# Kernel optimization log

Hardware: AMD Instinct MI355X
Metric: run time of the kernel (lower is better)

Reference implementation:

```python
import jax, jax.numpy as jnp
import numpy as np

N = 100000
E = 1600000
IN_C, HID_C, OUT_C = 128, 128, 64


def setup_inputs() -> dict:
    key = jax.random.key(0)
    k1, k2, k3, k4 = jax.random.split(key, 4)
    x = jax.random.normal(k1, (N, IN_C), dtype=jnp.float32)
    edge_index = jax.random.randint(k2, (2, E), 0, N, dtype=jnp.int32)
    # Glorot-ish scaled weights
    W1 = jax.random.normal(k3, (IN_C, HID_C), dtype=jnp.float32) / np.sqrt(IN_C)
    b1 = jnp.zeros((HID_C,), dtype=jnp.float32)
    W2 = jax.random.normal(k4, (HID_C, OUT_C), dtype=jnp.float32) / np.sqrt(HID_C)
    b2 = jnp.zeros((OUT_C,), dtype=jnp.float32)
    return {"x": x, "edge_index": edge_index, "W1": W1, "b1": b1, "W2": W2, "b2": b2}


def _gcn_norm(edge_index, num_nodes):
    """Add self loops and compute symmetric D^{-1/2} A D^{-1/2} edge weights (PyG GCNConv defaults)."""
    loop = jnp.arange(num_nodes, dtype=edge_index.dtype)
    row = jnp.concatenate([edge_index[0], loop])  # source nodes
    col = jnp.concatenate([edge_index[1], loop])  # target nodes
    ones = jnp.ones_like(col, dtype=jnp.float32)
    deg = jax.ops.segment_sum(ones, col, num_segments=num_nodes)
    deg_inv_sqrt = jnp.where(deg > 0, jax.lax.rsqrt(jnp.maximum(deg, 1.0)), 0.0)
    norm = deg_inv_sqrt[row] * deg_inv_sqrt[col]  # [E+N]
    return row, col, norm


def _gcn_layer(x, row, col, norm, W, b, num_nodes):
    h = x @ W                                   # [N, C_out] transform first (PyG order)
    msg = h[row] * norm[:, None]                # gather + scale  [E+N, C_out]
    out = jax.ops.segment_sum(msg, col, num_segments=num_nodes)  # scatter-add
    return out + b


def reference(x, edge_index, W1, b1, W2, b2):
    row, col, norm = _gcn_norm(edge_index, N)
    h = jax.nn.relu(_gcn_layer(x, row, col, norm, W1, b1, N))
    return _gcn_layer(h, row, col, norm, W2, b2, N)
```

## Files before the change

kernel.cpp:

```cpp
#include <hip/hip_runtime.h>
#include <hip/hip_fp16.h>

#define NODES 100000
#define EDGES 1600000

#define BSHIFT 9
#define BNODES 512
#define NBUCK ((NODES + BNODES - 1) / BNODES)
#define BCAP 10240

typedef __attribute__((ext_vector_type(8))) short short8;
typedef __attribute__((ext_vector_type(4))) float f32x4;

__device__ inline unsigned short f2bf(float f) {
    unsigned u = __builtin_bit_cast(unsigned, f);
    u = u + 0x7fff + ((u >> 16) & 1);
    return (unsigned short)(u >> 16);
}
__device__ inline float bf2f(unsigned short h) {
    unsigned u = ((unsigned)h) << 16;
    return __builtin_bit_cast(float, u);
}
__device__ inline unsigned short f2h_bits(float f) {
    __half h = __float2half_rn(f);
    return __builtin_bit_cast(unsigned short, h);
}
__device__ inline float h2f(unsigned short bits) {
    return __half2float(__builtin_bit_cast(__half, bits));
}
__device__ inline float2 h2f2(unsigned int bits) {
    __half2 h = __builtin_bit_cast(__half2, bits);
    return __half22float2(h);
}


__global__ __launch_bounds__(1024) void bucket_scatter(const int* __restrict__ row,
                                                       const int* __restrict__ col,
                                                       int* __restrict__ gcur,
                                                       int2* __restrict__ temp) {
    __shared__ int hist[NBUCK];
    __shared__ int base[NBUCK];
    const int tid = threadIdx.x;
    for (int i = tid; i < NBUCK; i += 1024) hist[i] = 0;
    __syncthreads();

    const int e = blockIdx.x * 1024 + tid;
    const bool valid = e < EDGES;
    int b = 0, rank = 0, src = 0, c = 0;
    if (valid) {
        c = col[e];
        src = row[e];
        b = c >> BSHIFT;
        rank = atomicAdd(&hist[b], 1);
    }
    __syncthreads();
    for (int i = tid; i < NBUCK; i += 1024) {
        int h = hist[i];
        base[i] = h ? atomicAdd(&gcur[i], h) : 0;
    }
    __syncthreads();
    if (valid) {
        int pos = base[b] + rank;
        int2 v;
        v.x = src;
        v.y = c & (BNODES - 1);
        temp[(size_t)b * BCAP + pos] = v;
    }
}

__global__ __launch_bounds__(256) void bucket_scan(const int* __restrict__ gcur,
                                                   int* __restrict__ bbase,
                                                   int* __restrict__ row_start) {
    __shared__ int s[256];
    const int t = threadIdx.x;
    int v = (t < NBUCK) ? gcur[t] : 0;
    s[t] = v;
    __syncthreads();
    for (int d = 1; d < 256; d <<= 1) {
        int x = (t >= d) ? s[t - d] : 0;
        __syncthreads();
        s[t] += x;
        __syncthreads();
    }
    if (t < NBUCK) bbase[t] = s[t] - v;
    if (t == 0) row_start[NODES] = EDGES;
}

__global__ __launch_bounds__(1024) void bucket_build(const int2* __restrict__ temp,
                                                     const int* __restrict__ gcur,
                                                     const int* __restrict__ bbase,
                                                     int* __restrict__ row_start,
                                                     float* __restrict__ dis,
                                                     int* __restrict__ esrc) {
    __shared__ int cnt[BNODES];
    __shared__ int offs[BNODES];
    __shared__ int cur[BNODES];
    const int b = blockIdx.x;
    const int tid = threadIdx.x;
    const int size = gcur[b];
    const int gbase = bbase[b];

    if (tid < BNODES) cnt[tid] = 0;
    __syncthreads();

    for (int i = tid; i < size; i += 1024) {
        int2 v = temp[(size_t)b * BCAP + i];
        atomicAdd(&cnt[v.y], 1);
    }
    __syncthreads();

    if (tid < BNODES) offs[tid] = cnt[tid];
    __syncthreads();
    for (int d = 1; d < BNODES; d <<= 1) {
        int x = 0;
        if (tid < BNODES && tid >= d) x = offs[tid - d];
        __syncthreads();
        if (tid < BNODES) offs[tid] += x;
        __syncthreads();
    }
    if (tid < BNODES) {
        int excl = offs[tid] - cnt[tid];
        cur[tid] = excl;
        int v = b * BNODES + tid;
        if (v < NODES) {
            row_start[v] = gbase + excl;
            dis[v] = rsqrtf((float)(cnt[tid] + 1));
        }
    }
    __syncthreads();

    for (int i = tid; i < size; i += 1024) {
        int2 v = temp[(size_t)b * BCAP + i];
        int pos = gbase + atomicAdd(&cur[v.y], 1);
        esrc[pos] = v.x;
    }
}


template <int NCOL>
__global__ __launch_bounds__(256) void w_prep(const float* __restrict__ W,
                                              unsigned short* __restrict__ wh,
                                              unsigned short* __restrict__ wl) {
    constexpr int NCT = NCOL / 16;
    constexpr int FRAGS = 4 * NCT * 64;
    int idx = blockIdx.x * 256 + threadIdx.x;
    if (idx >= FRAGS) return;
    int lane = idx & 63;
    int rem = idx >> 6;
    int ct = rem % NCT;
    int kt = rem / NCT;
    int kbase = kt * 32 + ((lane >> 4) * 8);
    int c = ct * 16 + (lane & 15);
#pragma unroll
    for (int i = 0; i < 8; i++) {
        float v = W[(size_t)(kbase + i) * NCOL + c];
        unsigned short hi = f2bf(v);
        unsigned short lo = f2bf(v - bf2f(hi));
        wh[(size_t)idx * 8 + i] = hi;
        wl[(size_t)idx * 8 + i] = lo;
    }
}


template <int NCOL, bool IN_HALF>
__global__ __launch_bounds__(512) void gemm_mfma(const void* __restrict__ Xv,
                                                 const unsigned short* __restrict__ wh,
                                                 const unsigned short* __restrict__ wl,
                                                 const float* __restrict__ dis,
                                                 unsigned short* __restrict__ H) {
    constexpr int NCT = NCOL / 16;
    constexpr int FRAGS = 4 * NCT * 64;
    __shared__ unsigned short s_wh[FRAGS * 8];
    __shared__ unsigned short s_wl[FRAGS * 8];

    const int tid = threadIdx.x;
    const int wave = tid >> 6;
    const int lane = tid & 63;

    const int row0 = blockIdx.x * 128 + wave * 16 + (lane & 15);
    const bool active = (blockIdx.x * 128 + wave * 16) < NODES;

    float xs[4][8];
    if (active) {
        if constexpr (IN_HALF) {
            const unsigned short* xrow = (const unsigned short*)Xv + (size_t)row0 * 128 + ((lane >> 4) * 8);
#pragma unroll
            for (int kt = 0; kt < 4; kt++) {
                short8 raw = *(const short8*)(xrow + kt * 32);
#pragma unroll
                for (int i = 0; i < 8; i++) xs[kt][i] = h2f((unsigned short)raw[i]);
            }
        } else {
            const float* xrow = (const float*)Xv + (size_t)row0 * 128 + ((lane >> 4) * 8);
#pragma unroll
            for (int kt = 0; kt < 4; kt++) {
                float4 a = *(const float4*)(xrow + kt * 32);
                float4 b = *(const float4*)(xrow + kt * 32 + 4);
                xs[kt][0] = a.x; xs[kt][1] = a.y; xs[kt][2] = a.z; xs[kt][3] = a.w;
                xs[kt][4] = b.x; xs[kt][5] = b.y; xs[kt][6] = b.z; xs[kt][7] = b.w;
            }
        }
    }

    constexpr int ROUNDS = (FRAGS * 16) / (512 * 16);
#pragma unroll
    for (int j = 0; j < ROUNDS; j++) {
        __builtin_amdgcn_global_load_lds((const unsigned int*)((const char*)wh + ((size_t)tid + j * 512) * 16),
                                         (unsigned int*)(s_wh + ((size_t)tid + j * 512) * 8), 16, 0, 0);
        __builtin_amdgcn_global_load_lds((const unsigned int*)((const char*)wl + ((size_t)tid + j * 512) * 16),
                                         (unsigned int*)(s_wl + ((size_t)tid + j * 512) * 8), 16, 0, 0);
    }
    __syncthreads();

    if (!active) return;

    short8 ah[4], al[4];
#pragma unroll
    for (int kt = 0; kt < 4; kt++) {
#pragma unroll
        for (int i = 0; i < 8; i++) {
            unsigned short hi = f2bf(xs[kt][i]);
            unsigned short lo = f2bf(xs[kt][i] - bf2f(hi));
            ah[kt][i] = (short)hi;
            al[kt][i] = (short)lo;
        }
    }

    f32x4 acc[NCT];
#pragma unroll
    for (int ct = 0; ct < NCT; ct++) acc[ct] = (f32x4){0.f, 0.f, 0.f, 0.f};

#pragma unroll
    for (int kt = 0; kt < 4; kt++) {
#pragma unroll
        for (int ct = 0; ct < NCT; ct++) {
            const int fo = ((kt * NCT + ct) * 64 + lane) * 8;
            short8 bh = *(const short8*)&s_wh[fo];
            short8 bl = *(const short8*)&s_wl[fo];
            acc[ct] = __builtin_amdgcn_mfma_f32_16x16x32_bf16(ah[kt], bh, acc[ct], 0, 0, 0);
            acc[ct] = __builtin_amdgcn_mfma_f32_16x16x32_bf16(al[kt], bh, acc[ct], 0, 0, 0);
            acc[ct] = __builtin_amdgcn_mfma_f32_16x16x32_bf16(ah[kt], bl, acc[ct], 0, 0, 0);
        }
    }

    const int rbase = blockIdx.x * 128 + wave * 16 + ((lane >> 4) * 4);
    float d[4];
#pragma unroll
    for (int r = 0; r < 4; r++) d[r] = dis[rbase + r];
#pragma unroll
    for (int ct = 0; ct < NCT; ct++) {
#pragma unroll
        for (int r = 0; r < 4; r++) {
            H[(size_t)(rbase + r) * NCOL + ct * 16 + (lane & 15)] = f2h_bits(acc[ct][r] * d[r]);
        }
    }
}


template <int C, bool RELU, bool OUT_HALF>
__global__ __launch_bounds__(256, 8) void agg_v3(const unsigned short* __restrict__ H,
                                                 const int* __restrict__ row_start,
                                                 const int* __restrict__ edge_src,
                                                 const float* __restrict__ dis,
                                                 const float* __restrict__ bias,
                                                 void* __restrict__ OUT) {
    constexpr int GL = (C == 128) ? 16 : 8;
    constexpr int GPW = 64 / GL;
    constexpr int RQ = C / 8;

    const int lane = threadIdx.x & 63;
    const int sub = lane & (GL - 1);
    const int grp = lane >> ((C == 128) ? 4 : 3);
    const int wid = (blockIdx.x * 256 + threadIdx.x) >> 6;
    const int v = wid * GPW + grp;
    if (v >= NODES) return;

    const uint4* __restrict__ Hq = (const uint4*)H;

    const int e0 = row_start[v];
    const int e1 = row_start[v + 1];
    const float d = dis[v];

    const float4 ba = ((const float4*)bias)[sub * 2];
    const float4 bb = ((const float4*)bias)[sub * 2 + 1];

    uint4 gs = Hq[(size_t)v * RQ + sub];

    int i0 = edge_src[min(e0 + 0, EDGES - 1)];
    int i1 = edge_src[min(e0 + 1, EDGES - 1)];
    int i2 = edge_src[min(e0 + 2, EDGES - 1)];
    int i3 = edge_src[min(e0 + 3, EDGES - 1)];

    float a0, a1, a2, a3, a4, a5, a6, a7;
    {
        float2 f0 = h2f2(gs.x), f1 = h2f2(gs.y), f2 = h2f2(gs.z), f3 = h2f2(gs.w);
        a0 = f0.x; a1 = f0.y; a2 = f1.x; a3 = f1.y;
        a4 = f2.x; a5 = f2.y; a6 = f3.x; a7 = f3.y;
    }

    for (int k = e0; k < e1; k += 4) {
        uint4 g0 = Hq[(size_t)i0 * RQ + sub];
        uint4 g1 = Hq[(size_t)i1 * RQ + sub];
        uint4 g2 = Hq[(size_t)i2 * RQ + sub];
        uint4 g3 = Hq[(size_t)i3 * RQ + sub];
        i0 = edge_src[min(k + 4, EDGES - 1)];
        i1 = edge_src[min(k + 5, EDGES - 1)];
        i2 = edge_src[min(k + 6, EDGES - 1)];
        i3 = edge_src[min(k + 7, EDGES - 1)];
        const float w1 = (k + 1 < e1) ? 1.f : 0.f;
        const float w2 = (k + 2 < e1) ? 1.f : 0.f;
        const float w3 = (k + 3 < e1) ? 1.f : 0.f;
#define ACC(G, W)                                                        \
        {                                                                \
            float2 f0 = h2f2(G.x), f1 = h2f2(G.y);                       \
            float2 f2 = h2f2(G.z), f3 = h2f2(G.w);                       \
            a0 = fmaf(f0.x, W, a0); a1 = fmaf(f0.y, W, a1);              \
            a2 = fmaf(f1.x, W, a2); a3 = fmaf(f1.y, W, a3);              \
            a4 = fmaf(f2.x, W, a4); a5 = fmaf(f2.y, W, a5);              \
            a6 = fmaf(f3.x, W, a6); a7 = fmaf(f3.y, W, a7);              \
        }
        ACC(g0, 1.f)
        ACC(g1, w1)
        ACC(g2, w2)
        ACC(g3, w3)
#undef ACC
    }

    float o0 = fmaf(a0, d, ba.x);
    float o1 = fmaf(a1, d, ba.y);
    float o2 = fmaf(a2, d, ba.z);
    float o3 = fmaf(a3, d, ba.w);
    float o4 = fmaf(a4, d, bb.x);
    float o5 = fmaf(a5, d, bb.y);
    float o6 = fmaf(a6, d, bb.z);
    float o7 = fmaf(a7, d, bb.w);
    if constexpr (RELU) {
        o0 = fmaxf(o0, 0.f); o1 = fmaxf(o1, 0.f);
        o2 = fmaxf(o2, 0.f); o3 = fmaxf(o3, 0.f);
        o4 = fmaxf(o4, 0.f); o5 = fmaxf(o5, 0.f);
        o6 = fmaxf(o6, 0.f); o7 = fmaxf(o7, 0.f);
    }

    if constexpr (OUT_HALF) {
        uint4 o;
        o.x = __builtin_bit_cast(unsigned, __float22half2_rn(make_float2(o0, o1)));
        o.y = __builtin_bit_cast(unsigned, __float22half2_rn(make_float2(o2, o3)));
        o.z = __builtin_bit_cast(unsigned, __float22half2_rn(make_float2(o4, o5)));
        o.w = __builtin_bit_cast(unsigned, __float22half2_rn(make_float2(o6, o7)));
        ((uint4*)OUT)[(size_t)v * RQ + sub] = o;
    } else {
        float4 oa, ob;
        oa.x = o0; oa.y = o1; oa.z = o2; oa.w = o3;
        ob.x = o4; ob.y = o5; ob.z = o6; ob.w = o7;
        float* outp = (float*)OUT + (size_t)v * C + sub * 8;
        *(float4*)(outp) = oa;
        *(float4*)(outp + 4) = ob;
    }
}


extern "C" void kernel_launch(void* const* d_in, const int* in_sizes, int n_in,
                              void* d_out, int out_size, void* d_ws, size_t ws_size,
                              hipStream_t stream) {
    const float* x   = (const float*)d_in[0];
    const int* eidx  = (const int*)d_in[1];
    const float* W1  = (const float*)d_in[2];
    const float* b1  = (const float*)d_in[3];
    const float* W2  = (const float*)d_in[4];
    const float* b2  = (const float*)d_in[5];
    float* out = (float*)d_out;

    const int* erow = eidx;
    const int* ecol = eidx + EDGES;

    char* w = (char*)d_ws;
    size_t off = 0;
    auto alloc = [&](size_t bytes) -> void* {
        void* p = w + off;
        off += (bytes + 255) & ~(size_t)255;
        return p;
    };
    float* dis     = (float*)alloc((size_t)NODES * 4);
    int*   rowst   = (int*)alloc((size_t)(NODES + 1) * 4);
    int*   esrc    = (int*)alloc((size_t)EDGES * 4);
    int*   gcur    = (int*)alloc(NBUCK * 4);
    int*   bbase   = (int*)alloc(NBUCK * 4);
    int2*  temp    = (int2*)alloc((size_t)NBUCK * BCAP * 8);
    unsigned short* wh1 = (unsigned short*)alloc(2048 * 8 * 2);
    unsigned short* wl1 = (unsigned short*)alloc(2048 * 8 * 2);
    unsigned short* wh2 = (unsigned short*)alloc(1024 * 8 * 2);
    unsigned short* wl2 = (unsigned short*)alloc(1024 * 8 * 2);
    unsigned short* bufA = (unsigned short*)alloc((size_t)NODES * 128 * 2);
    unsigned short* bufB = (unsigned short*)alloc((size_t)NODES * 128 * 2);

    hipMemsetAsync(gcur, 0, NBUCK * 4, stream);

    bucket_scatter<<<(EDGES + 1023) / 1024, 1024, 0, stream>>>(erow, ecol, gcur, temp);
    bucket_scan<<<1, 256, 0, stream>>>(gcur, bbase, rowst);
    bucket_build<<<NBUCK, 1024, 0, stream>>>(temp, gcur, bbase, rowst, dis, esrc);

    w_prep<128><<<8, 256, 0, stream>>>(W1, wh1, wl1);
    w_prep<64><<<4, 256, 0, stream>>>(W2, wh2, wl2);

    const int GB = (NODES + 127) / 128;

    gemm_mfma<128, false><<<GB, 512, 0, stream>>>(x, wh1, wl1, dis, bufA);
    agg_v3<128, true, true><<<(NODES + 15) / 16, 256, 0, stream>>>(bufA, rowst, esrc, dis, b1, bufB);

    gemm_mfma<64, true><<<GB, 512, 0, stream>>>(bufB, wh2, wl2, dis, bufA);
    agg_v3<64, false, false><<<(NODES + 31) / 32, 256, 0, stream>>>(bufA, rowst, esrc, dis, b2, out);
}
```

Before: 195.2 us.

## Fuse layer-1 aggregation with layer-2 matmul and merge small prep kernels

Fuses the layer-1 aggregation (with bias and ReLU) and the layer-2 weight transform into one kernel. The aggregated row is staged in LDS and multiplied by an fp16 copy of W2 using scalar FMAs, replacing the separate MFMA GEMM and its extra round trip of the hidden activations through HBM. Weight prep and the gcur zeroing are merged into one kernel, and the bucket scan is folded into every bucket_build block, removing several launches and the memset. The cost is per-block redundant scans and a scalar-FMA matvec, with W2 held in fp16 instead of split bf16 hi/lo, which lowers precision.

```diff
diff --git a/kernel.cpp b/kernel.cpp
--- a/kernel.cpp
+++ b/kernel.cpp
@@ -11,6 +11,7 @@
 
 typedef __attribute__((ext_vector_type(8))) short short8;
 typedef __attribute__((ext_vector_type(4))) float f32x4;
+typedef unsigned short ushort_t;
 
 __device__ inline unsigned short f2bf(float f) {
     unsigned u = __builtin_bit_cast(unsigned, f);
@@ -31,6 +32,42 @@
 __device__ inline float2 h2f2(unsigned int bits) {
     __half2 h = __builtin_bit_cast(__half2, bits);
     return __half22float2(h);
+}
+
+
+__global__ __launch_bounds__(256) void prep_kernel(const float* __restrict__ W1,
+                                                   const float* __restrict__ W2,
+                                                   unsigned short* __restrict__ wh,
+                                                   unsigned short* __restrict__ wl,
+                                                   unsigned short* __restrict__ w2h,
+                                                   int* __restrict__ gcur) {
+    const int tid = threadIdx.x;
+    if (blockIdx.x < 8) {
+        constexpr int NCOL = 128;
+        constexpr int NCT = NCOL / 16;
+        int idx = blockIdx.x * 256 + tid;
+        int lane = idx & 63;
+        int rem = idx >> 6;
+        int ct = rem % NCT;
+        int kt = rem / NCT;
+        int kbase = kt * 32 + ((lane >> 4) * 8);
+        int c = ct * 16 + (lane & 15);
+#pragma unroll
+        for (int i = 0; i < 8; i++) {
+            float v = W1[(size_t)(kbase + i) * NCOL + c];
+            unsigned short hi = f2bf(v);
+            unsigned short lo = f2bf(v - bf2f(hi));
+            wh[(size_t)idx * 8 + i] = hi;
+            wl[(size_t)idx * 8 + i] = lo;
+        }
+    } else {
+#pragma unroll
+        for (int i = 0; i < 32; i++) {
+            int idx = i * 256 + tid;
+            w2h[idx] = f2h_bits(W2[idx]);
+        }
+        if (tid < NBUCK) gcur[tid] = 0;
+    }
 }
 
 
@@ -68,37 +105,29 @@
     }
 }
 
-__global__ __launch_bounds__(256) void bucket_scan(const int* __restrict__ gcur,
-                                                   int* __restrict__ bbase,
-                                                   int* __restrict__ row_start) {
-    __shared__ int s[256];
-    const int t = threadIdx.x;
-    int v = (t < NBUCK) ? gcur[t] : 0;
-    s[t] = v;
-    __syncthreads();
-    for (int d = 1; d < 256; d <<= 1) {
-        int x = (t >= d) ? s[t - d] : 0;
-        __syncthreads();
-        s[t] += x;
-        __syncthreads();
-    }
-    if (t < NBUCK) bbase[t] = s[t] - v;
-    if (t == 0) row_start[NODES] = EDGES;
-}
-
 __global__ __launch_bounds__(1024) void bucket_build(const int2* __restrict__ temp,
                                                      const int* __restrict__ gcur,
-                                                     const int* __restrict__ bbase,
                                                      int* __restrict__ row_start,
                                                      float* __restrict__ dis,
                                                      int* __restrict__ esrc) {
     __shared__ int cnt[BNODES];
     __shared__ int offs[BNODES];
     __shared__ int cur[BNODES];
+    __shared__ int ssc[256];
     const int b = blockIdx.x;
     const int tid = threadIdx.x;
+
+    if (tid < 256) ssc[tid] = (tid < NBUCK) ? gcur[tid] : 0;
+    __syncthreads();
+    for (int d = 1; d < 256; d <<= 1) {
+        int x = (tid < 256 && tid >= d) ? ssc[tid - d] : 0;
+        __syncthreads();
+        if (tid < 256) ssc[tid] += x;
+        __syncthreads();
+    }
     const int size = gcur[b];
-    const int gbase = bbase[b];
+    const int gbase = ssc[b] - size;
+    if (b == 0 && tid == 0) row_start[NODES] = EDGES;
 
     if (tid < BNODES) cnt[tid] = 0;
     __syncthreads();
@@ -137,37 +166,12 @@
 }
 
 
-template <int NCOL>
-__global__ __launch_bounds__(256) void w_prep(const float* __restrict__ W,
-                                              unsigned short* __restrict__ wh,
-                                              unsigned short* __restrict__ wl) {
-    constexpr int NCT = NCOL / 16;
-    constexpr int FRAGS = 4 * NCT * 64;
-    int idx = blockIdx.x * 256 + threadIdx.x;
-    if (idx >= FRAGS) return;
-    int lane = idx & 63;
-    int rem = idx >> 6;
-    int ct = rem % NCT;
-    int kt = rem / NCT;
-    int kbase = kt * 32 + ((lane >> 4) * 8);
-    int c = ct * 16 + (lane & 15);
-#pragma unroll
-    for (int i = 0; i < 8; i++) {
-        float v = W[(size_t)(kbase + i) * NCOL + c];
-        unsigned short hi = f2bf(v);
-        unsigned short lo = f2bf(v - bf2f(hi));
-        wh[(size_t)idx * 8 + i] = hi;
-        wl[(size_t)idx * 8 + i] = lo;
-    }
-}
-
-
-template <int NCOL, bool IN_HALF>
-__global__ __launch_bounds__(512) void gemm_mfma(const void* __restrict__ Xv,
+__global__ __launch_bounds__(512) void gemm_mfma(const float* __restrict__ X,
                                                  const unsigned short* __restrict__ wh,
                                                  const unsigned short* __restrict__ wl,
                                                  const float* __restrict__ dis,
                                                  unsigned short* __restrict__ H) {
+    constexpr int NCOL = 128;
     constexpr int NCT = NCOL / 16;
     constexpr int FRAGS = 4 * NCT * 64;
     __shared__ unsigned short s_wh[FRAGS * 8];
@@ -182,23 +186,13 @@
 
     float xs[4][8];
     if (active) {
-        if constexpr (IN_HALF) {
-            const unsigned short* xrow = (const unsigned short*)Xv + (size_t)row0 * 128 + ((lane >> 4) * 8);
-#pragma unroll
-            for (int kt = 0; kt < 4; kt++) {
-                short8 raw = *(const short8*)(xrow + kt * 32);
-#pragma unroll
-                for (int i = 0; i < 8; i++) xs[kt][i] = h2f((unsigned short)raw[i]);
-            }
-        } else {
-            const float* xrow = (const float*)Xv + (size_t)row0 * 128 + ((lane >> 4) * 8);
-#pragma unroll
-            for (int kt = 0; kt < 4; kt++) {
-                float4 a = *(const float4*)(xrow + kt * 32);
-                float4 b = *(const float4*)(xrow + kt * 32 + 4);
-                xs[kt][0] = a.x; xs[kt][1] = a.y; xs[kt][2] = a.z; xs[kt][3] = a.w;
-                xs[kt][4] = b.x; xs[kt][5] = b.y; xs[kt][6] = b.z; xs[kt][7] = b.w;
-            }
+        const float* xrow = X + (size_t)row0 * 128 + ((lane >> 4) * 8);
+#pragma unroll
+        for (int kt = 0; kt < 4; kt++) {
+            float4 a = *(const float4*)(xrow + kt * 32);
+            float4 b = *(const float4*)(xrow + kt * 32 + 4);
+            xs[kt][0] = a.x; xs[kt][1] = a.y; xs[kt][2] = a.z; xs[kt][3] = a.w;
+            xs[kt][4] = b.x; xs[kt][5] = b.y; xs[kt][6] = b.z; xs[kt][7] = b.w;
         }
     }
 
@@ -257,23 +251,138 @@
 }
 
 
-template <int C, bool RELU, bool OUT_HALF>
-__global__ __launch_bounds__(256, 8) void agg_v3(const unsigned short* __restrict__ H,
+__global__ __launch_bounds__(256) void agg_fused(const unsigned short* __restrict__ H,
+                                                 const int* __restrict__ row_start,
+                                                 const int* __restrict__ edge_src,
+                                                 const float* __restrict__ dis,
+                                                 const float* __restrict__ b1,
+                                                 const unsigned short* __restrict__ w2h,
+                                                 unsigned short* __restrict__ H2) {
+    __shared__ float h_lds[16][128];
+    __shared__ unsigned short w2_lds[128 * 64];
+
+    const int tid = threadIdx.x;
+    const int lane = tid & 63;
+    const int sub = lane & 15;
+    const int grp = lane >> 4;
+    const int nl = (tid >> 6) * 4 + grp;
+    const int v = blockIdx.x * 16 + nl;
+
+#pragma unroll
+    for (int j = 0; j < 4; j++) {
+        __builtin_amdgcn_global_load_lds((const unsigned int*)((const char*)w2h + ((size_t)tid + j * 256) * 16),
+                                         (unsigned int*)w2_lds + ((size_t)tid + j * 256) * 4, 16, 0, 0);
+    }
+
+    const uint4* __restrict__ Hq = (const uint4*)H;
+    const int e0 = row_start[v];
+    const int e1 = row_start[v + 1];
+    const float d = dis[v];
+
+    const float4 ba = ((const float4*)b1)[sub * 2];
+    const float4 bb = ((const float4*)b1)[sub * 2 + 1];
+
+    uint4 gs = Hq[(size_t)v * 16 + sub];
+
+    int i0 = edge_src[min(e0 + 0, EDGES - 1)];
+    int i1 = edge_src[min(e0 + 1, EDGES - 1)];
+    int i2 = edge_src[min(e0 + 2, EDGES - 1)];
+    int i3 = edge_src[min(e0 + 3, EDGES - 1)];
+
+    float a0, a1, a2, a3, a4, a5, a6, a7;
+    {
+        float2 f0 = h2f2(gs.x), f1 = h2f2(gs.y), f2 = h2f2(gs.z), f3 = h2f2(gs.w);
+        a0 = f0.x; a1 = f0.y; a2 = f1.x; a3 = f1.y;
+        a4 = f2.x; a5 = f2.y; a6 = f3.x; a7 = f3.y;
+    }
+
+    for (int k = e0; k < e1; k += 4) {
+        uint4 g0 = Hq[(size_t)i0 * 16 + sub];
+        uint4 g1 = Hq[(size_t)i1 * 16 + sub];
+        uint4 g2 = Hq[(size_t)i2 * 16 + sub];
+        uint4 g3 = Hq[(size_t)i3 * 16 + sub];
+        i0 = edge_src[min(k + 4, EDGES - 1)];
+        i1 = edge_src[min(k + 5, EDGES - 1)];
+        i2 = edge_src[min(k + 6, EDGES - 1)];
+        i3 = edge_src[min(k + 7, EDGES - 1)];
+        const float w1 = (k + 1 < e1) ? 1.f : 0.f;
+        const float w2 = (k + 2 < e1) ? 1.f : 0.f;
+        const float w3 = (k + 3 < e1) ? 1.f : 0.f;
+#define ACC(G, W)                                                        \
+        {                                                                \
+            float2 f0 = h2f2(G.x), f1 = h2f2(G.y);                       \
+            float2 f2 = h2f2(G.z), f3 = h2f2(G.w);                       \
+            a0 = fmaf(f0.x, W, a0); a1 = fmaf(f0.y, W, a1);              \
+            a2 = fmaf(f1.x, W, a2); a3 = fmaf(f1.y, W, a3);              \
+            a4 = fmaf(f2.x, W, a4); a5 = fmaf(f2.y, W, a5);              \
+            a6 = fmaf(f3.x, W, a6); a7 = fmaf(f3.y, W, a7);              \
+        }
+        ACC(g0, 1.f)
+        ACC(g1, w1)
+        ACC(g2, w2)
+        ACC(g3, w3)
+#undef ACC
+    }
+
+    {
+        float4 oa, ob;
+        oa.x = fmaf(a0, d, ba.x); oa.y = fmaf(a1, d, ba.y);
+        oa.z = fmaf(a2, d, ba.z); oa.w = fmaf(a3, d, ba.w);
+        ob.x = fmaf(a4, d, bb.x); ob.y = fmaf(a5, d, bb.y);
+        ob.z = fmaf(a6, d, bb.z); ob.w = fmaf(a7, d, bb.w);
+        oa.x = fmaxf(oa.x, 0.f); oa.y = fmaxf(oa.y, 0.f);
+        oa.z = fmaxf(oa.z, 0.f); oa.w = fmaxf(oa.w, 0.f);
+        ob.x = fmaxf(ob.x, 0.f); ob.y = fmaxf(ob.y, 0.f);
+        ob.z = fmaxf(ob.z, 0.f); ob.w = fmaxf(ob.w, 0.f);
+        *(float4*)&h_lds[nl][sub * 8] = oa;
+        *(float4*)&h_lds[nl][sub * 8 + 4] = ob;
+    }
+    __syncthreads();
+
+    float c0 = 0.f, c1 = 0.f, c2 = 0.f, c3 = 0.f;
+#pragma unroll 8
+    for (int k4 = 0; k4 < 32; k4++) {
+        float4 s = *(const float4*)&h_lds[nl][k4 * 4];
+        const unsigned short* wrow = &w2_lds[(k4 * 4) * 64 + sub * 4];
+        uint2 w0 = *(const uint2*)(wrow);
+        uint2 w1 = *(const uint2*)(wrow + 64);
+        uint2 w2 = *(const uint2*)(wrow + 128);
+        uint2 w3 = *(const uint2*)(wrow + 192);
+#define MV(S, WW)                                                        \
+        {                                                                \
+            float2 p0 = h2f2(WW.x), p1 = h2f2(WW.y);                     \
+            c0 = fmaf(S, p0.x, c0); c1 = fmaf(S, p0.y, c1);              \
+            c2 = fmaf(S, p1.x, c2); c3 = fmaf(S, p1.y, c3);              \
+        }
+        MV(s.x, w0)
+        MV(s.y, w1)
+        MV(s.z, w2)
+        MV(s.w, w3)
+#undef MV
+    }
+
+    uint2 o;
+    o.x = __builtin_bit_cast(unsigned, __float22half2_rn(make_float2(c0 * d, c1 * d)));
+    o.y = __builtin_bit_cast(unsigned, __float22half2_rn(make_float2(c2 * d, c3 * d)));
+    ((uint2*)H2)[(size_t)v * 16 + sub] = o;
+}
+
+
+__global__ __launch_bounds__(256, 8) void agg_l2(const unsigned short* __restrict__ H,
                                                  const int* __restrict__ row_start,
                                                  const int* __restrict__ edge_src,
                                                  const float* __restrict__ dis,
                                                  const float* __restrict__ bias,
-                                                 void* __restrict__ OUT) {
-    constexpr int GL = (C == 128) ? 16 : 8;
-    constexpr int GPW = 64 / GL;
-    constexpr int RQ = C / 8;
+                                                 float* __restrict__ OUT) {
+    constexpr int GL = 8;
+    constexpr int GPW = 8;
+    constexpr int RQ = 8;
 
     const int lane = threadIdx.x & 63;
     const int sub = lane & (GL - 1);
-    const int grp = lane >> ((C == 128) ? 4 : 3);
+    const int grp = lane >> 3;
     const int wid = (blockIdx.x * 256 + threadIdx.x) >> 6;
     const int v = wid * GPW + grp;
-    if (v >= NODES) return;
 
     const uint4* __restrict__ Hq = (const uint4*)H;
 
@@ -326,36 +435,14 @@
 #undef ACC
     }
 
-    float o0 = fmaf(a0, d, ba.x);
-    float o1 = fmaf(a1, d, ba.y);
-    float o2 = fmaf(a2, d, ba.z);
-    float o3 = fmaf(a3, d, ba.w);
-    float o4 = fmaf(a4, d, bb.x);
-    float o5 = fmaf(a5, d, bb.y);
-    float o6 = fmaf(a6, d, bb.z);
-    float o7 = fmaf(a7, d, bb.w);
-    if constexpr (RELU) {
-        o0 = fmaxf(o0, 0.f); o1 = fmaxf(o1, 0.f);
-        o2 = fmaxf(o2, 0.f); o3 = fmaxf(o3, 0.f);
-        o4 = fmaxf(o4, 0.f); o5 = fmaxf(o5, 0.f);
-        o6 = fmaxf(o6, 0.f); o7 = fmaxf(o7, 0.f);
-    }
-
-    if constexpr (OUT_HALF) {
-        uint4 o;
-        o.x = __builtin_bit_cast(unsigned, __float22half2_rn(make_float2(o0, o1)));
-        o.y = __builtin_bit_cast(unsigned, __float22half2_rn(make_float2(o2, o3)));
-        o.z = __builtin_bit_cast(unsigned, __float22half2_rn(make_float2(o4, o5)));
-        o.w = __builtin_bit_cast(unsigned, __float22half2_rn(make_float2(o6, o7)));
-        ((uint4*)OUT)[(size_t)v * RQ + sub] = o;
-    } else {
-        float4 oa, ob;
-        oa.x = o0; oa.y = o1; oa.z = o2; oa.w = o3;
-        ob.x = o4; ob.y = o5; ob.z = o6; ob.w = o7;
-        float* outp = (float*)OUT + (size_t)v * C + sub * 8;
-        *(float4*)(outp) = oa;
-        *(float4*)(outp + 4) = ob;
-    }
+    float4 oa, ob;
+    oa.x = fmaf(a0, d, ba.x); oa.y = fmaf(a1, d, ba.y);
+    oa.z = fmaf(a2, d, ba.z); oa.w = fmaf(a3, d, ba.w);
+    ob.x = fmaf(a4, d, bb.x); ob.y = fmaf(a5, d, bb.y);
+    ob.z = fmaf(a6, d, bb.z); ob.w = fmaf(a7, d, bb.w);
+    float* outp = OUT + (size_t)v * 64 + sub * 8;
+    *(float4*)(outp) = oa;
+    *(float4*)(outp + 4) = ob;
 }
 
 
@@ -384,29 +471,22 @@
     int*   rowst   = (int*)alloc((size_t)(NODES + 1) * 4);
     int*   esrc    = (int*)alloc((size_t)EDGES * 4);
     int*   gcur    = (int*)alloc(NBUCK * 4);
-    int*   bbase   = (int*)alloc(NBUCK * 4);
     int2*  temp    = (int2*)alloc((size_t)NBUCK * BCAP * 8);
     unsigned short* wh1 = (unsigned short*)alloc(2048 * 8 * 2);
     unsigned short* wl1 = (unsigned short*)alloc(2048 * 8 * 2);
-    unsigned short* wh2 = (unsigned short*)alloc(1024 * 8 * 2);
-    unsigned short* wl2 = (unsigned short*)alloc(1024 * 8 * 2);
+    unsigned short* w2h = (unsigned short*)alloc(128 * 64 * 2);
     unsigned short* bufA = (unsigned short*)alloc((size_t)NODES * 128 * 2);
-    unsigned short* bufB = (unsigned short*)alloc((size_t)NODES * 128 * 2);
-
-    hipMemsetAsync(gcur, 0, NBUCK * 4, stream);
+    unsigned short* bufB = (unsigned short*)alloc((size_t)NODES * 64 * 2);
+
+    prep_kernel<<<9, 256, 0, stream>>>(W1, W2, wh1, wl1, w2h, gcur);
 
     bucket_scatter<<<(EDGES + 1023) / 1024, 1024, 0, stream>>>(erow, ecol, gcur, temp);
-    bucket_scan<<<1, 256, 0, stream>>>(gcur, bbase, rowst);
-    bucket_build<<<NBUCK, 1024, 0, stream>>>(temp, gcur, bbase, rowst, dis, esrc);
-
-    w_prep<128><<<8, 256, 0, stream>>>(W1, wh1, wl1);
-    w_prep<64><<<4, 256, 0, stream>>>(W2, wh2, wl2);
+    bucket_build<<<NBUCK, 1024, 0, stream>>>(temp, gcur, rowst, dis, esrc);
 
     const int GB = (NODES + 127) / 128;
-
-    gemm_mfma<128, false><<<GB, 512, 0, stream>>>(x, wh1, wl1, dis, bufA);
-    agg_v3<128, true, true><<<(NODES + 15) / 16, 256, 0, stream>>>(bufA, rowst, esrc, dis, b1, bufB);
-
-    gemm_mfma<64, true><<<GB, 512, 0, stream>>>(bufB, wh2, wl2, dis, bufA);
-    agg_v3<64, false, false><<<(NODES + 31) / 32, 256, 0, stream>>>(bufA, rowst, esrc, dis, b2, out);
-}
+    gemm_mfma<<<GB, 512, 0, stream>>>(x, wh1, wl1, dis, bufA);
+
+    agg_fused<<<NODES / 16, 256, 0, stream>>>(bufA, rowst, esrc, dis, b1, w2h, bufB);
+
+    agg_l2<<<NODES / 32, 256, 0, stream>>>(bufB, rowst, esrc, dis, b2, out);
+}
```

New measurement: 194.0 us. No clear change (-0.6%).

## Fuse edge bucketing with first GEMM and merge prep/scan kernels

Applied to the files above, without the earlier changes.

The first GEMM no longer depends on degree normalization, because the source-side dis scaling moves from the GEMM epilogue into the aggregation loop as a per-edge dis[src] gather. That lets the first GEMM run in the same launch as the edge bucket scatter, with extra blocks in one grid. Weight prep and the gcur zeroing are merged into a single small kernel, and the bucket scan is folded into every bucket_build block, which cuts launch count. The cost is an extra random dis gather per edge in both aggregation passes, and a 64KB shared-memory footprint shared by both block types in the fused kernel.

```diff
diff --git a/kernel.cpp b/kernel.cpp
--- a/kernel.cpp
+++ b/kernel.cpp
@@ -9,6 +9,9 @@
 #define NBUCK ((NODES + BNODES - 1) / BNODES)
 #define BCAP 10240
 
+#define GB 782
+#define SC 1563
+
 typedef __attribute__((ext_vector_type(8))) short short8;
 typedef __attribute__((ext_vector_type(4))) float f32x4;
 
@@ -34,71 +37,227 @@
 }
 
 
-__global__ __launch_bounds__(1024) void bucket_scatter(const int* __restrict__ row,
-                                                       const int* __restrict__ col,
-                                                       int* __restrict__ gcur,
-                                                       int2* __restrict__ temp) {
-    __shared__ int hist[NBUCK];
-    __shared__ int base[NBUCK];
+template <int NCOL>
+__device__ __forceinline__ void w_frag_prep(const float* __restrict__ W,
+                                            unsigned short* __restrict__ wh,
+                                            unsigned short* __restrict__ wl,
+                                            int idx) {
+    constexpr int NCT = NCOL / 16;
+    int lane = idx & 63;
+    int rem = idx >> 6;
+    int ct = rem % NCT;
+    int kt = rem / NCT;
+    int kbase = kt * 32 + ((lane >> 4) * 8);
+    int c = ct * 16 + (lane & 15);
+#pragma unroll
+    for (int i = 0; i < 8; i++) {
+        float v = W[(size_t)(kbase + i) * NCOL + c];
+        unsigned short hi = f2bf(v);
+        unsigned short lo = f2bf(v - bf2f(hi));
+        wh[(size_t)idx * 8 + i] = hi;
+        wl[(size_t)idx * 8 + i] = lo;
+    }
+}
+
+__global__ __launch_bounds__(256) void prep_kernel(const float* __restrict__ W1,
+                                                   const float* __restrict__ W2,
+                                                   unsigned short* __restrict__ wh1,
+                                                   unsigned short* __restrict__ wl1,
+                                                   unsigned short* __restrict__ wh2,
+                                                   unsigned short* __restrict__ wl2,
+                                                   int* __restrict__ gcur) {
     const int tid = threadIdx.x;
-    for (int i = tid; i < NBUCK; i += 1024) hist[i] = 0;
-    __syncthreads();
-
-    const int e = blockIdx.x * 1024 + tid;
-    const bool valid = e < EDGES;
-    int b = 0, rank = 0, src = 0, c = 0;
-    if (valid) {
-        c = col[e];
-        src = row[e];
-        b = c >> BSHIFT;
-        rank = atomicAdd(&hist[b], 1);
-    }
-    __syncthreads();
-    for (int i = tid; i < NBUCK; i += 1024) {
-        int h = hist[i];
-        base[i] = h ? atomicAdd(&gcur[i], h) : 0;
-    }
-    __syncthreads();
-    if (valid) {
-        int pos = base[b] + rank;
-        int2 v;
-        v.x = src;
-        v.y = c & (BNODES - 1);
-        temp[(size_t)b * BCAP + pos] = v;
-    }
-}
-
-__global__ __launch_bounds__(256) void bucket_scan(const int* __restrict__ gcur,
-                                                   int* __restrict__ bbase,
-                                                   int* __restrict__ row_start) {
-    __shared__ int s[256];
-    const int t = threadIdx.x;
-    int v = (t < NBUCK) ? gcur[t] : 0;
-    s[t] = v;
-    __syncthreads();
-    for (int d = 1; d < 256; d <<= 1) {
-        int x = (t >= d) ? s[t - d] : 0;
-        __syncthreads();
-        s[t] += x;
-        __syncthreads();
-    }
-    if (t < NBUCK) bbase[t] = s[t] - v;
-    if (t == 0) row_start[NODES] = EDGES;
-}
+    const int b = blockIdx.x;
+    if (b < 8) {
+        w_frag_prep<128>(W1, wh1, wl1, b * 256 + tid);
+    } else if (b < 12) {
+        w_frag_prep<64>(W2, wh2, wl2, (b - 8) * 256 + tid);
+    } else {
+        if (tid < NBUCK) gcur[tid] = 0;
+    }
+}
+
+
+template <int NCOL, bool IN_HALF>
+__device__ __forceinline__ void gemm_body(const void* __restrict__ Xv,
+                                          const unsigned short* __restrict__ wh,
+                                          const unsigned short* __restrict__ wl,
+                                          unsigned short* __restrict__ H,
+                                          unsigned short* s_wh,
+                                          unsigned short* s_wl,
+                                          int tid, int bid) {
+    constexpr int NCT = NCOL / 16;
+    constexpr int FRAGS = 4 * NCT * 64;
+
+    const int wave = tid >> 6;
+    const int lane = tid & 63;
+
+    const int row0 = bid * 128 + wave * 16 + (lane & 15);
+    const bool active = (bid * 128 + wave * 16) < NODES;
+
+    float xs[4][8];
+    if (active) {
+        if constexpr (IN_HALF) {
+            const unsigned short* xrow = (const unsigned short*)Xv + (size_t)row0 * 128 + ((lane >> 4) * 8);
+#pragma unroll
+            for (int kt = 0; kt < 4; kt++) {
+                short8 raw = *(const short8*)(xrow + kt * 32);
+#pragma unroll
+                for (int i = 0; i < 8; i++) xs[kt][i] = h2f((unsigned short)raw[i]);
+            }
+        } else {
+            const float* xrow = (const float*)Xv + (size_t)row0 * 128 + ((lane >> 4) * 8);
+#pragma unroll
+            for (int kt = 0; kt < 4; kt++) {
+                float4 a = *(const float4*)(xrow + kt * 32);
+                float4 b = *(const float4*)(xrow + kt * 32 + 4);
+                xs[kt][0] = a.x; xs[kt][1] = a.y; xs[kt][2] = a.z; xs[kt][3] = a.w;
+                xs[kt][4] = b.x; xs[kt][5] = b.y; xs[kt][6] = b.z; xs[kt][7] = b.w;
+            }
+        }
+    }
+
+    constexpr int ROUNDS = (FRAGS * 16) / (512 * 16);
+#pragma unroll
+    for (int j = 0; j < ROUNDS; j++) {
+        __builtin_amdgcn_global_load_lds((const unsigned int*)((const char*)wh + ((size_t)tid + j * 512) * 16),
+                                         (unsigned int*)(s_wh + ((size_t)tid + j * 512) * 8), 16, 0, 0);
+        __builtin_amdgcn_global_load_lds((const unsigned int*)((const char*)wl + ((size_t)tid + j * 512) * 16),
+                                         (unsigned int*)(s_wl + ((size_t)tid + j * 512) * 8), 16, 0, 0);
+    }
+    __syncthreads();
+
+    if (!active) return;
+
+    short8 ah[4], al[4];
+#pragma unroll
+    for (int kt = 0; kt < 4; kt++) {
+#pragma unroll
+        for (int i = 0; i < 8; i++) {
+            unsigned short hi = f2bf(xs[kt][i]);
+            unsigned short lo = f2bf(xs[kt][i] - bf2f(hi));
+            ah[kt][i] = (short)hi;
+            al[kt][i] = (short)lo;
+        }
+    }
+
+    f32x4 acc[NCT];
+#pragma unroll
+    for (int ct = 0; ct < NCT; ct++) acc[ct] = (f32x4){0.f, 0.f, 0.f, 0.f};
+
+#pragma unroll
+    for (int kt = 0; kt < 4; kt++) {
+#pragma unroll
+        for (int ct = 0; ct < NCT; ct++) {
+            const int fo = ((kt * NCT + ct) * 64 + lane) * 8;
+            short8 bh = *(const short8*)&s_wh[fo];
+            short8 bl = *(const short8*)&s_wl[fo];
+            acc[ct] = __builtin_amdgcn_mfma_f32_16x16x32_bf16(ah[kt], bh, acc[ct], 0, 0, 0);
+            acc[ct] = __builtin_amdgcn_mfma_f32_16x16x32_bf16(al[kt], bh, acc[ct], 0, 0, 0);
+            acc[ct] = __builtin_amdgcn_mfma_f32_16x16x32_bf16(ah[kt], bl, acc[ct], 0, 0, 0);
+        }
+    }
+
+    const int rbase = bid * 128 + wave * 16 + ((lane >> 4) * 4);
+#pragma unroll
+    for (int ct = 0; ct < NCT; ct++) {
+#pragma unroll
+        for (int r = 0; r < 4; r++) {
+            H[(size_t)(rbase + r) * NCOL + ct * 16 + (lane & 15)] = f2h_bits(acc[ct][r]);
+        }
+    }
+}
+
+
+__global__ __launch_bounds__(512) void gemm1_scatter(const float* __restrict__ X,
+                                                     const unsigned short* __restrict__ wh,
+                                                     const unsigned short* __restrict__ wl,
+                                                     unsigned short* __restrict__ H,
+                                                     const int* __restrict__ erow,
+                                                     const int* __restrict__ ecol,
+                                                     int* __restrict__ gcur,
+                                                     int2* __restrict__ temp) {
+    __shared__ __align__(16) char smem[65536];
+    const int tid = threadIdx.x;
+
+    if (blockIdx.x < GB) {
+        unsigned short* s_wh = (unsigned short*)smem;
+        unsigned short* s_wl = s_wh + 2048 * 8;
+        gemm_body<128, false>(X, wh, wl, H, s_wh, s_wl, tid, blockIdx.x);
+    } else {
+        int* hist = (int*)smem;
+        int* rbase = hist + NBUCK;
+        const int ebase = (blockIdx.x - GB) * 1024;
+        if (tid < NBUCK) hist[tid] = 0;
+        __syncthreads();
+
+        const int e0 = ebase + tid;
+        const int e1 = ebase + tid + 512;
+        const bool v0 = e0 < EDGES;
+        const bool v1 = e1 < EDGES;
+        int c0 = 0, s0 = 0, b0 = 0, r0 = 0;
+        int c1 = 0, s1 = 0, b1 = 0, r1 = 0;
+        if (v0) {
+            c0 = ecol[e0]; s0 = erow[e0];
+            b0 = c0 >> BSHIFT;
+            r0 = atomicAdd(&hist[b0], 1);
+        }
+        if (v1) {
+            c1 = ecol[e1]; s1 = erow[e1];
+            b1 = c1 >> BSHIFT;
+            r1 = atomicAdd(&hist[b1], 1);
+        }
+        __syncthreads();
+        if (tid < NBUCK) {
+            int h = hist[tid];
+            rbase[tid] = h ? atomicAdd(&gcur[tid], h) : 0;
+        }
+        __syncthreads();
+        if (v0) {
+            int2 v; v.x = s0; v.y = c0 & (BNODES - 1);
+            temp[(size_t)b0 * BCAP + rbase[b0] + r0] = v;
+        }
+        if (v1) {
+            int2 v; v.x = s1; v.y = c1 & (BNODES - 1);
+            temp[(size_t)b1 * BCAP + rbase[b1] + r1] = v;
+        }
+    }
+}
+
+
+__global__ __launch_bounds__(512) void gemm2_kernel(const unsigned short* __restrict__ X,
+                                                    const unsigned short* __restrict__ wh,
+                                                    const unsigned short* __restrict__ wl,
+                                                    unsigned short* __restrict__ H) {
+    __shared__ unsigned short s_wh[1024 * 8];
+    __shared__ unsigned short s_wl[1024 * 8];
+    gemm_body<64, true>(X, wh, wl, H, s_wh, s_wl, threadIdx.x, blockIdx.x);
+}
+
 
 __global__ __launch_bounds__(1024) void bucket_build(const int2* __restrict__ temp,
                                                      const int* __restrict__ gcur,
-                                                     const int* __restrict__ bbase,
                                                      int* __restrict__ row_start,
                                                      float* __restrict__ dis,
                                                      int* __restrict__ esrc) {
     __shared__ int cnt[BNODES];
     __shared__ int offs[BNODES];
     __shared__ int cur[BNODES];
+    __shared__ int ssc[256];
     const int b = blockIdx.x;
     const int tid = threadIdx.x;
+
+    if (tid < 256) ssc[tid] = (tid < NBUCK) ? gcur[tid] : 0;
+    __syncthreads();
+    for (int d = 1; d < 256; d <<= 1) {
+        int x = (tid < 256 && tid >= d) ? ssc[tid - d] : 0;
+        __syncthreads();
+        if (tid < 256) ssc[tid] += x;
+        __syncthreads();
+    }
     const int size = gcur[b];
-    const int gbase = bbase[b];
+    const int gbase = ssc[b] - size;
+    if (b == 0 && tid == 0) row_start[NODES] = EDGES;
 
     if (tid < BNODES) cnt[tid] = 0;
     __syncthreads();
@@ -137,128 +296,8 @@
 }
 
 
-template <int NCOL>
-__global__ __launch_bounds__(256) void w_prep(const float* __restrict__ W,
-                                              unsigned short* __restrict__ wh,
-                                              unsigned short* __restrict__ wl) {
-    constexpr int NCT = NCOL / 16;
-    constexpr int FRAGS = 4 * NCT * 64;
-    int idx = blockIdx.x * 256 + threadIdx.x;
-    if (idx >= FRAGS) return;
-    int lane = idx & 63;
-    int rem = idx >> 6;
-    int ct = rem % NCT;
-    int kt = rem / NCT;
-    int kbase = kt * 32 + ((lane >> 4) * 8);
-    int c = ct * 16 + (lane & 15);
-#pragma unroll
-    for (int i = 0; i < 8; i++) {
-        float v = W[(size_t)(kbase + i) * NCOL + c];
-        unsigned short hi = f2bf(v);
-        unsigned short lo = f2bf(v - bf2f(hi));
-        wh[(size_t)idx * 8 + i] = hi;
-        wl[(size_t)idx * 8 + i] = lo;
-    }
-}
-
-
-template <int NCOL, bool IN_HALF>
-__global__ __launch_bounds__(512) void gemm_mfma(const void* __restrict__ Xv,
-                                                 const unsigned short* __restrict__ wh,
-                                                 const unsigned short* __restrict__ wl,
-                                                 const float* __restrict__ dis,
-                                                 unsigned short* __restrict__ H) {
-    constexpr int NCT = NCOL / 16;
-    constexpr int FRAGS = 4 * NCT * 64;
-    __shared__ unsigned short s_wh[FRAGS * 8];
-    __shared__ unsigned short s_wl[FRAGS * 8];
-
-    const int tid = threadIdx.x;
-    const int wave = tid >> 6;
-    const int lane = tid & 63;
-
-    const int row0 = blockIdx.x * 128 + wave * 16 + (lane & 15);
-    const bool active = (blockIdx.x * 128 + wave * 16) < NODES;
-
-    float xs[4][8];
-    if (active) {
-        if constexpr (IN_HALF) {
-            const unsigned short* xrow = (const unsigned short*)Xv + (size_t)row0 * 128 + ((lane >> 4) * 8);
-#pragma unroll
-            for (int kt = 0; kt < 4; kt++) {
-                short8 raw = *(const short8*)(xrow + kt * 32);
-#pragma unroll
-                for (int i = 0; i < 8; i++) xs[kt][i] = h2f((unsigned short)raw[i]);
-            }
-        } else {
-            const float* xrow = (const float*)Xv + (size_t)row0 * 128 + ((lane >> 4) * 8);
-#pragma unroll
-            for (int kt = 0; kt < 4; kt++) {
-                float4 a = *(const float4*)(xrow + kt * 32);
-                float4 b = *(const float4*)(xrow + kt * 32 + 4);
-                xs[kt][0] = a.x; xs[kt][1] = a.y; xs[kt][2] = a.z; xs[kt][3] = a.w;
-                xs[kt][4] = b.x; xs[kt][5] = b.y; xs[kt][6] = b.z; xs[kt][7] = b.w;
-            }
-        }
-    }
-
-    constexpr int ROUNDS = (FRAGS * 16) / (512 * 16);
-#pragma unroll
-    for (int j = 0; j < ROUNDS; j++) {
-        __builtin_amdgcn_global_load_lds((const unsigned int*)((const char*)wh + ((size_t)tid + j * 512) * 16),
-                                         (unsigned int*)(s_wh + ((size_t)tid + j * 512) * 8), 16, 0, 0);
-        __builtin_amdgcn_global_load_lds((const unsigned int*)((const char*)wl + ((size_t)tid + j * 512) * 16),
-                                         (unsigned int*)(s_wl + ((size_t)tid + j * 512) * 8), 16, 0, 0);
-    }
-    __syncthreads();
-
-    if (!active) return;
-
-    short8 ah[4], al[4];
-#pragma unroll
-    for (int kt = 0; kt < 4; kt++) {
-#pragma unroll
-        for (int i = 0; i < 8; i++) {
-            unsigned short hi = f2bf(xs[kt][i]);
-            unsigned short lo = f2bf(xs[kt][i] - bf2f(hi));
-            ah[kt][i] = (short)hi;
-            al[kt][i] = (short)lo;
-        }
-    }
-
-    f32x4 acc[NCT];
-#pragma unroll
-    for (int ct = 0; ct < NCT; ct++) acc[ct] = (f32x4){0.f, 0.f, 0.f, 0.f};
-
-#pragma unroll
-    for (int kt = 0; kt < 4; kt++) {
-#pragma unroll
-        for (int ct = 0; ct < NCT; ct++) {
-            const int fo = ((kt * NCT + ct) * 64 + lane) * 8;
-            short8 bh = *(const short8*)&s_wh[fo];
-            short8 bl = *(const short8*)&s_wl[fo];
-            acc[ct] = __builtin_amdgcn_mfma_f32_16x16x32_bf16(ah[kt], bh, acc[ct], 0, 0, 0);
-            acc[ct] = __builtin_amdgcn_mfma_f32_16x16x32_bf16(al[kt], bh, acc[ct], 0, 0, 0);
-            acc[ct] = __builtin_amdgcn_mfma_f32_16x16x32_bf16(ah[kt], bl, acc[ct], 0, 0, 0);
-        }
-    }
-
-    const int rbase = blockIdx.x * 128 + wave * 16 + ((lane >> 4) * 4);
-    float d[4];
-#pragma unroll
-    for (int r = 0; r < 4; r++) d[r] = dis[rbase + r];
-#pragma unroll
-    for (int ct = 0; ct < NCT; ct++) {
-#pragma unroll
-        for (int r = 0; r < 4; r++) {
-            H[(size_t)(rbase + r) * NCOL + ct * 16 + (lane & 15)] = f2h_bits(acc[ct][r] * d[r]);
-        }
-    }
-}
-
-
 template <int C, bool RELU, bool OUT_HALF>
-__global__ __launch_bounds__(256, 8) void agg_v3(const unsigned short* __restrict__ H,
+__global__ __launch_bounds__(256, 8) void agg_v4(const unsigned short* __restrict__ H,
                                                  const int* __restrict__ row_start,
                                                  const int* __restrict__ edge_src,
                                                  const float* __restrict__ dis,
@@ -279,7 +318,7 @@
 
     const int e0 = row_start[v];
     const int e1 = row_start[v + 1];
-    const float d = dis[v];
+    const float dv = dis[v];
 
     const float4 ba = ((const float4*)bias)[sub * 2];
     const float4 bb = ((const float4*)bias)[sub * 2 + 1];
@@ -290,12 +329,13 @@
     int i1 = edge_src[min(e0 + 1, EDGES - 1)];
     int i2 = edge_src[min(e0 + 2, EDGES - 1)];
     int i3 = edge_src[min(e0 + 3, EDGES - 1)];
+    float d0 = dis[i0], d1 = dis[i1], d2 = dis[i2], d3 = dis[i3];
 
     float a0, a1, a2, a3, a4, a5, a6, a7;
     {
         float2 f0 = h2f2(gs.x), f1 = h2f2(gs.y), f2 = h2f2(gs.z), f3 = h2f2(gs.w);
-        a0 = f0.x; a1 = f0.y; a2 = f1.x; a3 = f1.y;
-        a4 = f2.x; a5 = f2.y; a6 = f3.x; a7 = f3.y;
+        a0 = f0.x * dv; a1 = f0.y * dv; a2 = f1.x * dv; a3 = f1.y * dv;
+        a4 = f2.x * dv; a5 = f2.y * dv; a6 = f3.x * dv; a7 = f3.y * dv;
     }
 
     for (int k = e0; k < e1; k += 4) {
@@ -303,13 +343,15 @@
         uint4 g1 = Hq[(size_t)i1 * RQ + sub];
         uint4 g2 = Hq[(size_t)i2 * RQ + sub];
         uint4 g3 = Hq[(size_t)i3 * RQ + sub];
-        i0 = edge_src[min(k + 4, EDGES - 1)];
-        i1 = edge_src[min(k + 5, EDGES - 1)];
-        i2 = edge_src[min(k + 6, EDGES - 1)];
-        i3 = edge_src[min(k + 7, EDGES - 1)];
-        const float w1 = (k + 1 < e1) ? 1.f : 0.f;
-        const float w2 = (k + 2 < e1) ? 1.f : 0.f;
-        const float w3 = (k + 3 < e1) ? 1.f : 0.f;
+        const int n0 = edge_src[min(k + 4, EDGES - 1)];
+        const int n1 = edge_src[min(k + 5, EDGES - 1)];
+        const int n2 = edge_src[min(k + 6, EDGES - 1)];
+        const int n3 = edge_src[min(k + 7, EDGES - 1)];
+        const float dn0 = dis[n0], dn1 = dis[n1], dn2 = dis[n2], dn3 = dis[n3];
+        const float w0 = d0;
+        const float w1 = (k + 1 < e1) ? d1 : 0.f;
+        const float w2 = (k + 2 < e1) ? d2 : 0.f;
+        const float w3 = (k + 3 < e1) ? d3 : 0.f;
 #define ACC(G, W)                                                        \
         {                                                                \
             float2 f0 = h2f2(G.x), f1 = h2f2(G.y);                       \
@@ -319,21 +361,23 @@
             a4 = fmaf(f2.x, W, a4); a5 = fmaf(f2.y, W, a5);              \
             a6 = fmaf(f3.x, W, a6); a7 = fmaf(f3.y, W, a7);              \
         }
-        ACC(g0, 1.f)
+        ACC(g0, w0)
         ACC(g1, w1)
         ACC(g2, w2)
         ACC(g3, w3)
 #undef ACC
-    }
-
-    float o0 = fmaf(a0, d, ba.x);
-    float o1 = fmaf(a1, d, ba.y);
-    float o2 = fmaf(a2, d, ba.z);
-    float o3 = fmaf(a3, d, ba.w);
-    float o4 = fmaf(a4, d, bb.x);
-    float o5 = fmaf(a5, d, bb.y);
-    float o6 = fmaf(a6, d, bb.z);
-    float o7 = fmaf(a7, d, bb.w);
+        i0 = n0; i1 = n1; i2 = n2; i3 = n3;
+        d0 = dn0; d1 = dn1; d2 = dn2; d3 = dn3;
+    }
+
+    float o0 = fmaf(a0, dv, ba.x);
+    float o1 = fmaf(a1, dv, ba.y);
+    float o2 = fmaf(a2, dv, ba.z);
+    float o3 = fmaf(a3, dv, ba.w);
+    float o4 = fmaf(a4, dv, bb.x);
+    float o5 = fmaf(a5, dv, bb.y);
+    float o6 = fmaf(a6, dv, bb.z);
+    float o7 = fmaf(a7, dv, bb.w);
     if constexpr (RELU) {
         o0 = fmaxf(o0, 0.f); o1 = fmaxf(o1, 0.f);
         o2 = fmaxf(o2, 0.f); o3 = fmaxf(o3, 0.f);
@@ -384,7 +428,6 @@
     int*   rowst   = (int*)alloc((size_t)(NODES + 1) * 4);
     int*   esrc    = (int*)alloc((size_t)EDGES * 4);
     int*   gcur    = (int*)alloc(NBUCK * 4);
-    int*   bbase   = (int*)alloc(NBUCK * 4);
     int2*  temp    = (int2*)alloc((size_t)NBUCK * BCAP * 8);
     unsigned short* wh1 = (unsigned short*)alloc(2048 * 8 * 2);
     unsigned short* wl1 = (unsigned short*)alloc(2048 * 8 * 2);
@@ -392,21 +435,17 @@
     unsigned short* wl2 = (unsigned short*)alloc(1024 * 8 * 2);
     unsigned short* bufA = (unsigned short*)alloc((size_t)NODES * 128 * 2);
     unsigned short* bufB = (unsigned short*)alloc((size_t)NODES * 128 * 2);
-
-    hipMemsetAsync(gcur, 0, NBUCK * 4, stream);
-
-    bucket_scatter<<<(EDGES + 1023) / 1024, 1024, 0, stream>>>(erow, ecol, gcur, temp);
-    bucket_scan<<<1, 256, 0, stream>>>(gcur, bbase, rowst);
-    bucket_build<<<NBUCK, 1024, 0, stream>>>(temp, gcur, bbase, rowst, dis, esrc);
-
-    w_prep<128><<<8, 256, 0, stream>>>(W1, wh1, wl1);
-    w_prep<64><<<4, 256, 0, stream>>>(W2, wh2, wl2);
-
-    const int GB = (NODES + 127) / 128;
-
-    gemm_mfma<128, false><<<GB, 512, 0, stream>>>(x, wh1, wl1, dis, bufA);
-    agg_v3<128, true, true><<<(NODES + 15) / 16, 256, 0, stream>>>(bufA, rowst, esrc, dis, b1, bufB);
-
-    gemm_mfma<64, true><<<GB, 512, 0, stream>>>(bufB, wh2, wl2, dis, bufA);
-    agg_v3<64, false, false><<<(NODES + 31) / 32, 256, 0, stream>>>(bufA, rowst, esrc, dis, b2, out);
-}
+    unsigned short* bufC = (unsigned short*)alloc((size_t)NODES * 64 * 2);
+
+    prep_kernel<<<13, 256, 0, stream>>>(W1, W2, wh1, wl1, wh2, wl2, gcur);
+
+    gemm1_scatter<<<GB + SC, 512, 0, stream>>>(x, wh1, wl1, bufA, erow, ecol, gcur, temp);
+
+    bucket_build<<<NBUCK, 1024, 0, stream>>>(temp, gcur, rowst, dis, esrc);
+
+    agg_v4<128, true, true><<<NODES / 16, 256, 0, stream>>>(bufA, rowst, esrc, dis, b1, bufB);
+
+    gemm2_kernel<<<GB, 512, 0, stream>>>(bufB, wh2, wl2, bufC);
+
+    agg_v4<64, false, false><<<NODES / 32, 256, 0, stream>>>(bufC, rowst, esrc, dis, b2, out);
+}
```

After: 184.6 us. 1.06x faster.
